# Kernel optimization log

Measured on AMD Instinct MI355X. Metric: run time of the kernel, lower is better.

## Reference

```python
import jax, jax.numpy as jnp
import numpy as np

B, D, H, E, TOPK = 8192, 1024, 4096, 8, 2


def setup_inputs() -> dict:
    key = jax.random.key(0)
    ks = jax.random.split(key, 5)
    s_in = 1.0 / np.sqrt(D)
    s_h = 1.0 / np.sqrt(H)
    return {
        "x": jax.random.normal(ks[0], (B, D), jnp.float32),
        "Wg": jax.random.normal(ks[1], (D, E), jnp.float32) * s_in,
        "bg": jnp.zeros((E,), jnp.float32),
        "W1": jax.random.normal(ks[2], (E, D, H), jnp.float32) * s_in,
        "b1": jnp.zeros((E, H), jnp.float32),
        "W2": jax.random.normal(ks[3], (E, H, D), jnp.float32) * s_h,
        "b2": jnp.zeros((E, D), jnp.float32),
    }


def reference(x, Wg, bg, W1, b1, W2, b2):
    # Gating: softmax over experts, top-k, renormalize selected weights
    logits = x @ Wg + bg                              # [B, E]
    weights = jax.nn.softmax(logits, axis=-1)
    topw, topi = jax.lax.top_k(weights, TOPK)         # [B, k]
    topw = topw / jnp.sum(topw, axis=-1, keepdims=True)
    # Dense combine weights: [B, E], zero for unselected experts
    comb = jnp.sum(topw[..., None] * jax.nn.one_hot(topi, E, dtype=x.dtype), axis=1)
    # Expert MLPs computed batched per expert (grouped GEMM form)
    h = jax.nn.gelu(jnp.einsum('bd,edh->ebh', x, W1) + b1[:, None, :], approximate=False)  # [E,B,H]
    y = jnp.einsum('ebh,ehd->ebd', h, W2) + b2[:, None, :]                                 # [E,B,D]
    # Weighted combine: only top-k experts have nonzero weight
    out = jnp.einsum('ebd,be->bd', y, comb)           # [B, D]
    return out
```

## Files before the change

kernel.cpp:

```cpp
#include <hip/hip_runtime.h>
#include <stdint.h>

#define B_TOK 8192
#define DDIM 1024
#define HDIM 4096
#define NEXP 8
#define MAXTILE 72

typedef __bf16 bf16x8 __attribute__((ext_vector_type(8)));
typedef float f32x4 __attribute__((ext_vector_type(4)));

__device__ __forceinline__ unsigned short f2bf(float f) {
  unsigned int u = __float_as_uint(f);
  u += 0x7fffu + ((u >> 16) & 1u);
  return (unsigned short)(u >> 16);
}
__device__ __forceinline__ float bfhi(unsigned int u) {
  return __uint_as_float(u & 0xffff0000u);
}
__device__ __forceinline__ float bflo(unsigned int u) {
  return __uint_as_float(u << 16);
}

__device__ __forceinline__ void gld16(const void* g, void* l) {
  __builtin_amdgcn_global_load_lds(
      (const __attribute__((address_space(1))) void*)g,
      (__attribute__((address_space(3))) void*)l, 16, 0, 0);
}

__device__ __forceinline__ float gelu_f(float v) {
  float u = v * (0.7978845608f + 0.0356774081f * v * v);
  float ex = __expf(2.f * u);
  float th = 1.f - 2.f * __builtin_amdgcn_rcpf(ex + 1.f);
  return 0.5f * v * (1.f + th);
}

__global__ __launch_bounds__(256) void gating_kernel(
    const float* __restrict__ x, const float* __restrict__ Wg,
    const float* __restrict__ bg, int* __restrict__ t2e,
    float* __restrict__ t2w, int* __restrict__ cnt) {
  __shared__ float sWg[NEXP * DDIM];
  int tid = threadIdx.x;
  for (int i = tid; i < NEXP * DDIM; i += 256) {
    int d = i >> 3, e = i & 7;
    sWg[e * DDIM + d] = Wg[i];
  }
  __syncthreads();
  int lane = tid & 63, wave = tid >> 6;
  for (int t = 0; t < 16; ++t) {
    int b = blockIdx.x * 64 + wave * 16 + t;
    float acc[NEXP];
#pragma unroll
    for (int e = 0; e < NEXP; ++e) acc[e] = 0.f;
    const float* xr = x + (size_t)b * DDIM;
#pragma unroll
    for (int j = 0; j < 4; ++j) {
      int d0 = j * 256 + lane * 4;
      float4 xv = *(const float4*)(xr + d0);
#pragma unroll
      for (int e = 0; e < NEXP; ++e) {
        float4 wv = *(const float4*)(sWg + e * DDIM + d0);
        acc[e] += xv.x * wv.x + xv.y * wv.y + xv.z * wv.z + xv.w * wv.w;
      }
    }
#pragma unroll
    for (int off = 32; off > 0; off >>= 1) {
#pragma unroll
      for (int e = 0; e < NEXP; ++e) acc[e] += __shfl_xor(acc[e], off);
    }
    if (lane == 0) {
      float l0[NEXP];
#pragma unroll
      for (int e = 0; e < NEXP; ++e) l0[e] = acc[e] + bg[e];
      int i1 = 0;
      float v1 = l0[0];
#pragma unroll
      for (int e = 1; e < NEXP; ++e)
        if (l0[e] > v1) { v1 = l0[e]; i1 = e; }
      int i2 = (i1 == 0) ? 1 : 0;
      float v2 = l0[i2];
#pragma unroll
      for (int e = 0; e < NEXP; ++e)
        if (e != i1 && l0[e] > v2) { v2 = l0[e]; i2 = e; }
      float w1 = 1.f / (1.f + expf(v2 - v1));
      float w2 = 1.f - w1;
      t2e[b * 2] = i1;
      t2e[b * 2 + 1] = i2;
      t2w[b * 2] = w1;
      t2w[b * 2 + 1] = w2;
      atomicAdd(&cnt[i1], 1);
      atomicAdd(&cnt[i2], 1);
    }
  }
}

__global__ void prefix_kernel(const int* __restrict__ cnt, int* __restrict__ offs,
                              int* __restrict__ tileE, int* __restrict__ tileM,
                              int* __restrict__ ntile) {
  int s = 0, t = 0;
  offs[0] = 0;
  for (int e = 0; e < NEXP; ++e) {
    int c = cnt[e];
    for (int m = 0; m < c; m += 256) { tileE[t] = e; tileM[t] = m; ++t; }
    s += c;
    offs[e + 1] = s;
  }
  *ntile = t;
}

__global__ __launch_bounds__(256) void scatter_kernel(
    const int* __restrict__ t2e, const int* __restrict__ offs,
    int* __restrict__ cursor, int* __restrict__ tok, int* __restrict__ rowpos) {
  int b = blockIdx.x * 256 + threadIdx.x;
  if (b >= B_TOK) return;
#pragma unroll
  for (int k = 0; k < 2; ++k) {
    int e = t2e[b * 2 + k];
    int pos = offs[e] + atomicAdd(&cursor[e], 1);
    tok[pos] = b;
    rowpos[b * 2 + k] = pos;
  }
}

__global__ __launch_bounds__(256) void cvt_x_kernel(const float* __restrict__ x,
                                                    unsigned short* __restrict__ xb) {
  size_t i = ((size_t)blockIdx.x * 256 + threadIdx.x) * 4;
  float4 v = *(const float4*)(x + i);
  ushort4 o;
  o.x = f2bf(v.x);
  o.y = f2bf(v.y);
  o.z = f2bf(v.z);
  o.w = f2bf(v.w);
  *(ushort4*)(xb + i) = o;
}

__global__ __launch_bounds__(256) void transpose_cvt_kernel(
    const float* __restrict__ src, unsigned short* __restrict__ dst, int R, int C) {
  __shared__ unsigned short T[64][72];
  size_t eo = (size_t)blockIdx.z * (size_t)R * C;
  int c0 = blockIdx.x * 64, r0 = blockIdx.y * 64;
  int tid = threadIdx.x;
#pragma unroll
  for (int p = 0; p < 4; ++p) {
    int idx = p * 256 + tid;
    int r = idx >> 4, c4 = (idx & 15) * 4;
    float4 v = *(const float4*)(src + eo + (size_t)(r0 + r) * C + c0 + c4);
    T[r][c4] = f2bf(v.x);
    T[r][c4 + 1] = f2bf(v.y);
    T[r][c4 + 2] = f2bf(v.z);
    T[r][c4 + 3] = f2bf(v.w);
  }
  __syncthreads();
#pragma unroll
  for (int p = 0; p < 2; ++p) {
    int idx = p * 256 + tid;
    int c = idx >> 3, s8 = (idx & 7) * 8;
    ushort4 a, b;
    a.x = T[s8][c];     a.y = T[s8 + 1][c]; a.z = T[s8 + 2][c]; a.w = T[s8 + 3][c];
    b.x = T[s8 + 4][c]; b.y = T[s8 + 5][c]; b.z = T[s8 + 6][c]; b.w = T[s8 + 7][c];
    unsigned short* dp = dst + eo + (size_t)(c0 + c) * R + r0 + s8;
    *(ushort4*)dp = a;
    *(ushort4*)(dp + 4) = b;
  }
}

#define BAR() __builtin_amdgcn_s_barrier()
#define LG0() asm volatile("s_waitcnt lgkmcnt(0)" ::: "memory")
#define VM6() asm volatile("s_waitcnt vmcnt(6)" ::: "memory")
#define VM0() asm volatile("s_waitcnt vmcnt(0)" ::: "memory")
#define RGN(t, mat, ks) (&LDS[(t) & 1][mat][ks][0][0])
#define STAGE(mat, P0, P1, t, ks)                                   \
  do {                                                              \
    unsigned short* _d = RGN(t, mat, ks) + wave * 512;              \
    gld16((P0) + (size_t)(t) * 64 + (ks) * 32, _d);                 \
    gld16((P1) + (size_t)(t) * 64 + (ks) * 32, _d + 4096);          \
  } while (0)
#define RDA(t, ks)                                                  \
  do {                                                              \
    const unsigned short* _p = RGN(t, 0, ks);                       \
    _Pragma("unroll") for (int n = 0; n < 4; ++n)                   \
        a[n] = *(const bf16x8*)(_p + aoff[n]);                      \
  } while (0)
#define RDB(t, ks, h)                                               \
  do {                                                              \
    const unsigned short* _p = RGN(t, 1, ks);                       \
    _Pragma("unroll") for (int m = 0; m < 4; ++m)                   \
        b[m] = *(const bf16x8*)(_p + boff2[h][m]);                  \
  } while (0)
#define MMQ(h)                                                      \
  do {                                                              \
    __builtin_amdgcn_s_setprio(1);                                  \
    _Pragma("unroll") for (int i = 0; i < 4; ++i)                   \
        _Pragma("unroll") for (int j = 0; j < 4; ++j)               \
            acc[i][(h)*4 + j] = __builtin_amdgcn_mfma_f32_16x16x32_bf16( \
                a[i], b[j], acc[i][(h)*4 + j], 0, 0, 0);            \
    __builtin_amdgcn_s_setprio(0);                                  \
  } while (0)

template <int KD, bool GELU, bool GATHER>
__global__ __launch_bounds__(512, 2) void moe_gemm(
    const unsigned short* __restrict__ Bsrc, const unsigned short* __restrict__ Wt,
    const float* __restrict__ bias, const int* __restrict__ offs,
    const int* __restrict__ tileE, const int* __restrict__ tileM,
    const int* __restrict__ ntile, const int* __restrict__ tok,
    unsigned short* __restrict__ obuf, int ND) {
  constexpr int NT = KD / 64;
  __shared__ __attribute__((aligned(16))) unsigned short LDS[2][2][2][256][32];
  int ty = blockIdx.y;
  if (ty >= *ntile) return;
  int e = tileE[ty], m0 = tileM[ty];
  int r0 = offs[e], rows = offs[e + 1] - r0;
  int n0 = blockIdx.x * 256;
  int tid = threadIdx.x, lane = tid & 63, wave = tid >> 6;
  int wn = wave & 3, wm = wave >> 2;
  int nbase = wn * 64, mbase = wm * 128;
  int fr = lane & 15, quad = lane >> 4;

  int rs = tid >> 2;
  int ss = (tid & 3) ^ ((rs >> 1) & 3);
  const unsigned short* pA0 = Wt + ((size_t)e * ND + n0 + rs) * KD + ss * 8;
  const unsigned short* pA1 = pA0 + (size_t)128 * KD;
  int mr0 = min(m0 + rs, rows - 1), mr1 = min(m0 + 128 + rs, rows - 1);
  size_t br0, br1;
  if constexpr (GATHER) {
    br0 = (size_t)tok[r0 + mr0];
    br1 = (size_t)tok[r0 + mr1];
  } else {
    br0 = (size_t)(r0 + mr0);
    br1 = (size_t)(r0 + mr1);
  }
  const unsigned short* pB0 = Bsrc + br0 * KD + ss * 8;
  const unsigned short* pB1 = Bsrc + br1 * KD + ss * 8;

  int aoff[4], boff2[2][4];
#pragma unroll
  for (int n = 0; n < 4; ++n) {
    int rA = nbase + n * 16 + fr;
    aoff[n] = rA * 32 + (quad ^ ((rA >> 1) & 3)) * 8;
  }
#pragma unroll
  for (int h = 0; h < 2; ++h)
#pragma unroll
    for (int m = 0; m < 4; ++m) {
      int rB = mbase + h * 64 + m * 16 + fr;
      boff2[h][m] = rB * 32 + (quad ^ ((rB >> 1) & 3)) * 8;
    }

  f32x4 acc[4][8];
#pragma unroll
  for (int i = 0; i < 4; ++i)
#pragma unroll
    for (int j = 0; j < 8; ++j) acc[i][j] = (f32x4){0.f, 0.f, 0.f, 0.f};
  bf16x8 a[4], b[4];

  STAGE(0, pA0, pA1, 0, 0);
  STAGE(1, pB0, pB1, 0, 0);
  STAGE(0, pA0, pA1, 0, 1);
  STAGE(1, pB0, pB1, 0, 1);
  STAGE(0, pA0, pA1, 1, 0);
  STAGE(1, pB0, pB1, 1, 0);
  STAGE(0, pA0, pA1, 1, 1);
  VM6();
  BAR();

  for (int t = 0; t < NT - 2; ++t) {
    RDA(t, 0); RDB(t, 0, 0);
    STAGE(1, pB0, pB1, t + 1, 1);
    BAR(); LG0();
    MMQ(0);
    BAR();
    RDB(t, 0, 1);
    STAGE(0, pA0, pA1, t + 2, 0);
    BAR(); LG0();
    MMQ(1);
    BAR();
    RDA(t, 1); RDB(t, 1, 0);
    STAGE(1, pB0, pB1, t + 2, 0);
    BAR(); LG0();
    MMQ(0);
    BAR();
    RDB(t, 1, 1);
    STAGE(0, pA0, pA1, t + 2, 1);
    VM6();
    BAR(); LG0();
    MMQ(1);
    BAR();
  }
  {
    int t = NT - 2;
    RDA(t, 0); RDB(t, 0, 0);
    STAGE(1, pB0, pB1, t + 1, 1);
    BAR(); LG0();
    MMQ(0);
    BAR();
    RDB(t, 0, 1);
    BAR(); LG0();
    MMQ(1);
    BAR();
    RDA(t, 1); RDB(t, 1, 0);
    BAR(); LG0();
    MMQ(0);
    BAR();
    RDB(t, 1, 1);
    VM0();
    BAR(); LG0();
    MMQ(1);
    BAR();
  }
  {
    int t = NT - 1;
    RDA(t, 0); RDB(t, 0, 0);
    BAR(); LG0();
    MMQ(0);
    BAR();
    RDB(t, 0, 1);
    BAR(); LG0();
    MMQ(1);
    BAR();
    RDA(t, 1); RDB(t, 1, 0);
    BAR(); LG0();
    MMQ(0);
    BAR();
    RDB(t, 1, 1);
    LG0();
    MMQ(1);
  }

  const float* be = bias + (size_t)e * ND + n0 + nbase;
  float4 bv[4];
#pragma unroll
  for (int i = 0; i < 4; ++i) bv[i] = *(const float4*)(be + i * 16 + quad * 4);
#pragma unroll
  for (int j = 0; j < 8; ++j) {
    int grow = m0 + mbase + (j >> 2) * 64 + (j & 3) * 16 + fr;
    if (grow < rows) {
      unsigned short* yp = obuf + (size_t)(r0 + grow) * ND + n0 + nbase;
#pragma unroll
      for (int i = 0; i < 4; ++i) {
        float v0 = acc[i][j][0] + bv[i].x;
        float v1 = acc[i][j][1] + bv[i].y;
        float v2 = acc[i][j][2] + bv[i].z;
        float v3 = acc[i][j][3] + bv[i].w;
        if constexpr (GELU) {
          v0 = gelu_f(v0); v1 = gelu_f(v1); v2 = gelu_f(v2); v3 = gelu_f(v3);
        }
        ushort4 o;
        o.x = f2bf(v0); o.y = f2bf(v1); o.z = f2bf(v2); o.w = f2bf(v3);
        *(ushort4*)(yp + i * 16 + quad * 4) = o;
      }
    }
  }
}

__global__ __launch_bounds__(256) void combine_kernel(
    const unsigned short* __restrict__ ybuf, const int* __restrict__ rowpos,
    const float* __restrict__ t2w, float* __restrict__ out) {
  int idx = blockIdx.x * 256 + threadIdx.x;
  int b = idx >> 7;
  int c8 = (idx & 127) * 8;
  int p0 = rowpos[b * 2], p1 = rowpos[b * 2 + 1];
  float w0 = t2w[b * 2], w1 = t2w[b * 2 + 1];
  uint4 ya = *(const uint4*)(ybuf + (size_t)p0 * DDIM + c8);
  uint4 yb = *(const uint4*)(ybuf + (size_t)p1 * DDIM + c8);
  float4 o0, o1;
  o0.x = w0 * bflo(ya.x) + w1 * bflo(yb.x);
  o0.y = w0 * bfhi(ya.x) + w1 * bfhi(yb.x);
  o0.z = w0 * bflo(ya.y) + w1 * bflo(yb.y);
  o0.w = w0 * bfhi(ya.y) + w1 * bfhi(yb.y);
  o1.x = w0 * bflo(ya.z) + w1 * bflo(yb.z);
  o1.y = w0 * bfhi(ya.z) + w1 * bfhi(yb.z);
  o1.z = w0 * bflo(ya.w) + w1 * bflo(yb.w);
  o1.w = w0 * bfhi(ya.w) + w1 * bfhi(yb.w);
  float* op = out + (size_t)b * DDIM + c8;
  *(float4*)op = o0;
  *(float4*)(op + 4) = o1;
}

extern "C" void kernel_launch(void* const* d_in, const int* in_sizes, int n_in,
                              void* d_out, int out_size, void* d_ws, size_t ws_size,
                              hipStream_t stream) {
  const float* x = (const float*)d_in[0];
  const float* Wg = (const float*)d_in[1];
  const float* bg = (const float*)d_in[2];
  const float* W1 = (const float*)d_in[3];
  const float* b1 = (const float*)d_in[4];
  const float* W2 = (const float*)d_in[5];
  const float* b2 = (const float*)d_in[6];
  float* out = (float*)d_out;

  char* ws = (char*)d_ws;
  int* cnt = (int*)(ws + 0);
  int* cursor = (int*)(ws + 64);
  int* offs = (int*)(ws + 128);
  int* ntile = (int*)(ws + 192);
  int* tileE = (int*)(ws + 256);
  int* tileM = (int*)(ws + 896);
  int* t2e = (int*)(ws + 2048);
  float* t2w = (float*)(ws + 67584);
  int* tok = (int*)(ws + 133120);
  int* rowpos = (int*)(ws + 198656);
  char* big = ws + 264192;
  unsigned short* xb = (unsigned short*)big;
  unsigned short* w1t = (unsigned short*)(big + 16777216);
  unsigned short* ybuf = w1t;
  unsigned short* w2t = (unsigned short*)(big + 16777216 + 67108864);
  unsigned short* hbuf = (unsigned short*)(big + 16777216 + 2 * 67108864);

  (void)in_sizes; (void)n_in; (void)out_size; (void)ws_size;

  hipMemsetAsync(ws, 0, 256, stream);

  cvt_x_kernel<<<(B_TOK * DDIM) / 1024, 256, 0, stream>>>(x, xb);
  transpose_cvt_kernel<<<dim3(HDIM / 64, DDIM / 64, NEXP), 256, 0, stream>>>(W1, w1t, DDIM, HDIM);
  transpose_cvt_kernel<<<dim3(DDIM / 64, HDIM / 64, NEXP), 256, 0, stream>>>(W2, w2t, HDIM, DDIM);
  gating_kernel<<<B_TOK / 64, 256, 0, stream>>>(x, Wg, bg, t2e, t2w, cnt);
  prefix_kernel<<<1, 1, 0, stream>>>(cnt, offs, tileE, tileM, ntile);
  scatter_kernel<<<B_TOK / 256, 256, 0, stream>>>(t2e, offs, cursor, tok, rowpos);
  moe_gemm<DDIM, true, true><<<dim3(HDIM / 256, MAXTILE), 512, 0, stream>>>(
      xb, w1t, b1, offs, tileE, tileM, ntile, tok, hbuf, HDIM);
  moe_gemm<HDIM, false, false><<<dim3(DDIM / 256, MAXTILE), 512, 0, stream>>>(
      hbuf, w2t, b2, offs, tileE, tileM, ntile, tok, ybuf, DDIM);
  combine_kernel<<<(B_TOK * DDIM) / (256 * 8), 256, 0, stream>>>(ybuf, rowpos, t2w, out);
}
```

Baseline: 993.6 us.

## Double-buffer MFMA fragments in MoE GEMM, fuse x conversion into gating, batch scatter atomics

The GEMM main loop now uses two sets of A/B register fragments, so LDS reads for the next quarter-step are issued before the current MFMA block and the barrier waits are relaxed. Scheduling barriers pin the instruction order and the vmcnt thresholds are retuned. The bf16 conversion of x moves into the gating kernel, which already reads x, so one kernel launch and one full read of x go away. The scatter kernel now counts per expert in LDS and does one global atomic per expert per block instead of one per token. The cost is higher register pressure from the extra fragment sets, and the tighter wait counts are easy to get wrong.

```diff
diff --git a/kernel.cpp b/kernel.cpp
--- a/kernel.cpp
+++ b/kernel.cpp
@@ -38,7 +38,8 @@
 __global__ __launch_bounds__(256) void gating_kernel(
     const float* __restrict__ x, const float* __restrict__ Wg,
     const float* __restrict__ bg, int* __restrict__ t2e,
-    float* __restrict__ t2w, int* __restrict__ cnt) {
+    float* __restrict__ t2w, int* __restrict__ cnt,
+    unsigned short* __restrict__ xb) {
   __shared__ float sWg[NEXP * DDIM];
   int tid = threadIdx.x;
   for (int i = tid; i < NEXP * DDIM; i += 256) {
@@ -53,10 +54,14 @@
 #pragma unroll
     for (int e = 0; e < NEXP; ++e) acc[e] = 0.f;
     const float* xr = x + (size_t)b * DDIM;
+    unsigned short* xw = xb + (size_t)b * DDIM;
 #pragma unroll
     for (int j = 0; j < 4; ++j) {
       int d0 = j * 256 + lane * 4;
       float4 xv = *(const float4*)(xr + d0);
+      ushort4 o;
+      o.x = f2bf(xv.x); o.y = f2bf(xv.y); o.z = f2bf(xv.z); o.w = f2bf(xv.w);
+      *(ushort4*)(xw + d0) = o;
 #pragma unroll
       for (int e = 0; e < NEXP; ++e) {
         float4 wv = *(const float4*)(sWg + e * DDIM + d0);
@@ -111,27 +116,23 @@
 __global__ __launch_bounds__(256) void scatter_kernel(
     const int* __restrict__ t2e, const int* __restrict__ offs,
     int* __restrict__ cursor, int* __restrict__ tok, int* __restrict__ rowpos) {
-  int b = blockIdx.x * 256 + threadIdx.x;
-  if (b >= B_TOK) return;
-#pragma unroll
-  for (int k = 0; k < 2; ++k) {
-    int e = t2e[b * 2 + k];
-    int pos = offs[e] + atomicAdd(&cursor[e], 1);
-    tok[pos] = b;
-    rowpos[b * 2 + k] = pos;
-  }
-}
-
-__global__ __launch_bounds__(256) void cvt_x_kernel(const float* __restrict__ x,
-                                                    unsigned short* __restrict__ xb) {
-  size_t i = ((size_t)blockIdx.x * 256 + threadIdx.x) * 4;
-  float4 v = *(const float4*)(x + i);
-  ushort4 o;
-  o.x = f2bf(v.x);
-  o.y = f2bf(v.y);
-  o.z = f2bf(v.z);
-  o.w = f2bf(v.w);
-  *(ushort4*)(xb + i) = o;
+  __shared__ int lcnt[NEXP], lbase[NEXP];
+  int tid = threadIdx.x;
+  if (tid < NEXP) lcnt[tid] = 0;
+  __syncthreads();
+  int b = blockIdx.x * 256 + tid;
+  int e0 = t2e[b * 2], e1 = t2e[b * 2 + 1];
+  int i0 = atomicAdd(&lcnt[e0], 1);
+  int i1 = atomicAdd(&lcnt[e1], 1);
+  __syncthreads();
+  if (tid < NEXP) lbase[tid] = atomicAdd(&cursor[tid], lcnt[tid]);
+  __syncthreads();
+  int p0 = offs[e0] + lbase[e0] + i0;
+  int p1 = offs[e1] + lbase[e1] + i1;
+  tok[p0] = b;
+  tok[p1] = b;
+  rowpos[b * 2] = p0;
+  rowpos[b * 2 + 1] = p1;
 }
 
 __global__ __launch_bounds__(256) void transpose_cvt_kernel(
@@ -165,35 +166,35 @@
 }
 
 #define BAR() __builtin_amdgcn_s_barrier()
+#define SB() __builtin_amdgcn_sched_barrier(0)
 #define LG0() asm volatile("s_waitcnt lgkmcnt(0)" ::: "memory")
-#define VM6() asm volatile("s_waitcnt vmcnt(6)" ::: "memory")
-#define VM0() asm volatile("s_waitcnt vmcnt(0)" ::: "memory")
+#define VMW(n) asm volatile("s_waitcnt vmcnt(" #n ")" ::: "memory")
 #define RGN(t, mat, ks) (&LDS[(t) & 1][mat][ks][0][0])
-#define STAGE(mat, P0, P1, t, ks)                                   \
+#define STAGE(mat, P0p, P1p, t, ks)                                 \
   do {                                                              \
     unsigned short* _d = RGN(t, mat, ks) + wave * 512;              \
-    gld16((P0) + (size_t)(t) * 64 + (ks) * 32, _d);                 \
-    gld16((P1) + (size_t)(t) * 64 + (ks) * 32, _d + 4096);          \
+    gld16((P0p) + (size_t)(t) * 64 + (ks) * 32, _d);                \
+    gld16((P1p) + (size_t)(t) * 64 + (ks) * 32, _d + 4096);         \
   } while (0)
-#define RDA(t, ks)                                                  \
+#define RDA_TO(dst, t, ks)                                          \
   do {                                                              \
     const unsigned short* _p = RGN(t, 0, ks);                       \
     _Pragma("unroll") for (int n = 0; n < 4; ++n)                   \
-        a[n] = *(const bf16x8*)(_p + aoff[n]);                      \
+        dst[n] = *(const bf16x8*)(_p + aoff[n]);                    \
   } while (0)
-#define RDB(t, ks, h)                                               \
+#define RDB_TO(dst, t, ks, h)                                       \
   do {                                                              \
     const unsigned short* _p = RGN(t, 1, ks);                       \
     _Pragma("unroll") for (int m = 0; m < 4; ++m)                   \
-        b[m] = *(const bf16x8*)(_p + boff2[h][m]);                  \
+        dst[m] = *(const bf16x8*)(_p + boff2[h][m]);                \
   } while (0)
-#define MMQ(h)                                                      \
+#define MMQ2(Av, Bv, h)                                             \
   do {                                                              \
     __builtin_amdgcn_s_setprio(1);                                  \
     _Pragma("unroll") for (int i = 0; i < 4; ++i)                   \
         _Pragma("unroll") for (int j = 0; j < 4; ++j)               \
             acc[i][(h)*4 + j] = __builtin_amdgcn_mfma_f32_16x16x32_bf16( \
-                a[i], b[j], acc[i][(h)*4 + j], 0, 0, 0);            \
+                Av[i], Bv[j], acc[i][(h)*4 + j], 0, 0, 0);          \
     __builtin_amdgcn_s_setprio(0);                                  \
   } while (0)
 
@@ -205,6 +206,7 @@
     const int* __restrict__ ntile, const int* __restrict__ tok,
     unsigned short* __restrict__ obuf, int ND) {
   constexpr int NT = KD / 64;
+  static_assert(NT >= 3, "pipeline needs >=3 K-tiles");
   __shared__ __attribute__((aligned(16))) unsigned short LDS[2][2][2][256][32];
   int ty = blockIdx.y;
   if (ty >= *ntile) return;
@@ -251,7 +253,7 @@
   for (int i = 0; i < 4; ++i)
 #pragma unroll
     for (int j = 0; j < 8; ++j) acc[i][j] = (f32x4){0.f, 0.f, 0.f, 0.f};
-  bf16x8 a[4], b[4];
+  bf16x8 aE[4], aO[4], bE[4], bO[4];
 
   STAGE(0, pA0, pA1, 0, 0);
   STAGE(1, pB0, pB1, 0, 0);
@@ -260,70 +262,83 @@
   STAGE(0, pA0, pA1, 1, 0);
   STAGE(1, pB0, pB1, 1, 0);
   STAGE(0, pA0, pA1, 1, 1);
-  VM6();
+  VMW(10);
   BAR();
+  RDA_TO(aE, 0, 0);
+  RDB_TO(bE, 0, 0, 0);
+  LG0();
+  SB();
 
   for (int t = 0; t < NT - 2; ++t) {
-    RDA(t, 0); RDB(t, 0, 0);
+    RDB_TO(bO, t, 0, 1);
     STAGE(1, pB0, pB1, t + 1, 1);
-    BAR(); LG0();
-    MMQ(0);
-    BAR();
-    RDB(t, 0, 1);
+    SB();
+    MMQ2(aE, bE, 0);
+    SB();
+    VMW(8); LG0(); SB();
+    BAR();
+    RDA_TO(aO, t, 1);
+    RDB_TO(bE, t, 1, 0);
     STAGE(0, pA0, pA1, t + 2, 0);
-    BAR(); LG0();
-    MMQ(1);
-    BAR();
-    RDA(t, 1); RDB(t, 1, 0);
+    SB();
+    MMQ2(aE, bO, 1);
+    SB();
+    LG0(); SB();
+    BAR();
+    RDB_TO(bO, t, 1, 1);
     STAGE(1, pB0, pB1, t + 2, 0);
-    BAR(); LG0();
-    MMQ(0);
-    BAR();
-    RDB(t, 1, 1);
+    SB();
+    MMQ2(aO, bE, 0);
+    SB();
+    VMW(8); LG0(); SB();
+    BAR();
+    RDA_TO(aE, t + 1, 0);
+    RDB_TO(bE, t + 1, 0, 0);
     STAGE(0, pA0, pA1, t + 2, 1);
-    VM6();
-    BAR(); LG0();
-    MMQ(1);
+    SB();
+    MMQ2(aO, bO, 1);
+    SB();
+    LG0(); SB();
     BAR();
   }
   {
     int t = NT - 2;
-    RDA(t, 0); RDB(t, 0, 0);
+    RDB_TO(bO, t, 0, 1);
     STAGE(1, pB0, pB1, t + 1, 1);
-    BAR(); LG0();
-    MMQ(0);
-    BAR();
-    RDB(t, 0, 1);
-    BAR(); LG0();
-    MMQ(1);
-    BAR();
-    RDA(t, 1); RDB(t, 1, 0);
-    BAR(); LG0();
-    MMQ(0);
-    BAR();
-    RDB(t, 1, 1);
-    VM0();
-    BAR(); LG0();
-    MMQ(1);
+    SB(); MMQ2(aE, bE, 0); SB();
+    VMW(8); LG0(); SB();
+    BAR();
+    RDA_TO(aO, t, 1);
+    RDB_TO(bE, t, 1, 0);
+    SB(); MMQ2(aE, bO, 1); SB();
+    LG0(); SB();
+    BAR();
+    RDB_TO(bO, t, 1, 1);
+    SB(); MMQ2(aO, bE, 0); SB();
+    VMW(4); LG0(); SB();
+    BAR();
+    RDA_TO(aE, t + 1, 0);
+    RDB_TO(bE, t + 1, 0, 0);
+    SB(); MMQ2(aO, bO, 1); SB();
+    LG0(); SB();
     BAR();
   }
   {
     int t = NT - 1;
-    RDA(t, 0); RDB(t, 0, 0);
-    BAR(); LG0();
-    MMQ(0);
-    BAR();
-    RDB(t, 0, 1);
-    BAR(); LG0();
-    MMQ(1);
-    BAR();
-    RDA(t, 1); RDB(t, 1, 0);
-    BAR(); LG0();
-    MMQ(0);
-    BAR();
-    RDB(t, 1, 1);
-    LG0();
-    MMQ(1);
+    RDB_TO(bO, t, 0, 1);
+    SB(); MMQ2(aE, bE, 0); SB();
+    VMW(0); LG0(); SB();
+    BAR();
+    RDA_TO(aO, t, 1);
+    RDB_TO(bE, t, 1, 0);
+    SB(); MMQ2(aE, bO, 1); SB();
+    LG0(); SB();
+    BAR();
+    RDB_TO(bO, t, 1, 1);
+    SB(); MMQ2(aO, bE, 0); SB();
+    LG0(); SB();
+    BAR();
+    SB(); MMQ2(aO, bO, 1); SB();
   }
 
   const float* be = bias + (size_t)e * ND + n0 + nbase;
@@ -410,10 +425,9 @@
 
   hipMemsetAsync(ws, 0, 256, stream);
 
-  cvt_x_kernel<<<(B_TOK * DDIM) / 1024, 256, 0, stream>>>(x, xb);
   transpose_cvt_kernel<<<dim3(HDIM / 64, DDIM / 64, NEXP), 256, 0, stream>>>(W1, w1t, DDIM, HDIM);
   transpose_cvt_kernel<<<dim3(DDIM / 64, HDIM / 64, NEXP), 256, 0, stream>>>(W2, w2t, HDIM, DDIM);
-  gating_kernel<<<B_TOK / 64, 256, 0, stream>>>(x, Wg, bg, t2e, t2w, cnt);
+  gating_kernel<<<B_TOK / 64, 256, 0, stream>>>(x, Wg, bg, t2e, t2w, cnt, xb);
   prefix_kernel<<<1, 1, 0, stream>>>(cnt, offs, tileE, tileM, ntile);
   scatter_kernel<<<B_TOK / 256, 256, 0, stream>>>(t2e, offs, cursor, tok, rowpos);
   moe_gemm<DDIM, true, true><<<dim3(HDIM / 256, MAXTILE), 512, 0, stream>>>(
```

After: 904.3 us. 1.1x faster.
